# Performance work log

Measured on AMD Instinct MI355X. Metric: run time of the kernel, lower is better.

Reference implementation:

```python
import jax, jax.numpy as jnp
import numpy as np

N = 1024      # node_dim
D = 1024      # initial_dim (== node_dim so all QRs are square)
B = 8         # batch_dim
L = 4         # layer_dim
DEG = 16      # out-degree per node
E = N * DEG


def setup_inputs() -> dict:
    key = jax.random.key(0)
    k1, k2 = jax.random.split(key)
    x0 = jax.random.normal(k1, (B, N, D), dtype=jnp.float32)
    # every node appears as a source exactly DEG times -> degree > 0 everywhere
    src = jnp.repeat(jnp.arange(N, dtype=jnp.int64), DEG)
    dst = jax.random.randint(k2, (E,), 0, N, dtype=jnp.int64)
    edge_index = jnp.stack([src, dst], axis=1)
    return {"x0": x0, "edge_index": edge_index, "run": 1}


def _rfp_conv(x, src, dst, deg):
    # x: [N, D]; one RFPConv application on a single graph signal
    inv_sqrt = deg ** -0.5                               # deg^{-1/2}
    w = inv_sqrt[src] * inv_sqrt[dst]                    # [E]
    msg = w[:, None] * x[dst]                            # gathered + normalized neighbour feats
    agg = 0.5 * jax.ops.segment_sum(msg, src, num_segments=N)
    # unsorted_segment_mean(deg[src]*x[src], src) == sum / count, count = deg
    src_term = deg[src][:, None] * x[src]
    mean = jax.ops.segment_sum(src_term, src, num_segments=N) / jnp.maximum(deg, 1.0)[:, None]
    agg = agg + 0.5 * mean                               # [N, D]
    # D == N so reduced QR == complete (full_matrices=True) QR
    return jnp.linalg.qr(agg)[0]


def reference(x0, edge_index, run):
    if not run:
        return None
    src = edge_index[:, 0]
    dst = edge_index[:, 1]
    deg = jax.ops.segment_sum(jnp.ones((E,), jnp.float32), src, num_segments=N)
    conv = jax.vmap(lambda x: _rfp_conv(x, src, dst, deg))
    traj = [x0]
    for i in range(L):
        traj.append(conv(traj[i]))
    return jnp.concatenate(traj, axis=-1)  # [B, N, D + L*N]
```

## Files before the change

kernel.cpp:

```cpp
#include <hip/hip_runtime.h>
#include <cmath>

#define NN 1024
#define DD 1024
#define BB 8
#define LL 4
#define OUTD (DD*(LL+1))
#define NB 32
#define NPAN 32
#define BSTR ((size_t)NN*OUTD)
#define VSTR 540672ull

typedef short b8v __attribute__((ext_vector_type(8)));
typedef float f4v __attribute__((ext_vector_type(4)));

__device__ __forceinline__ unsigned short f2bf(float x){
  unsigned u=__float_as_uint(x);
  return (unsigned short)((u + 0x7FFFu + ((u>>16)&1u))>>16);
}
__device__ __forceinline__ float bf2f(unsigned short h){
  return __uint_as_float(((unsigned)h)<<16);
}
__device__ __forceinline__ void bsplit3(float x, short& h, short& m, short& l){
  unsigned short hh=f2bf(x);
  float r1=x-bf2f(hh);
  unsigned short mm=f2bf(r1);
  float r2=r1-bf2f(mm);
  h=(short)hh; m=(short)mm; l=(short)f2bf(r2);
}
__device__ __forceinline__ f4v mfma6(b8v ah,b8v am,b8v al,b8v bh,b8v bm,b8v bl,f4v acc){
  acc=__builtin_amdgcn_mfma_f32_16x16x32_bf16(al,bh,acc,0,0,0);
  acc=__builtin_amdgcn_mfma_f32_16x16x32_bf16(ah,bl,acc,0,0,0);
  acc=__builtin_amdgcn_mfma_f32_16x16x32_bf16(am,bm,acc,0,0,0);
  acc=__builtin_amdgcn_mfma_f32_16x16x32_bf16(am,bh,acc,0,0,0);
  acc=__builtin_amdgcn_mfma_f32_16x16x32_bf16(ah,bm,acc,0,0,0);
  acc=__builtin_amdgcn_mfma_f32_16x16x32_bf16(ah,bh,acc,0,0,0);
  return acc;
}
__device__ __forceinline__ size_t voff(int kb){
  return 32768ull*(size_t)kb - 512ull*(size_t)kb*(size_t)(kb-1);
}

__device__ __forceinline__ void wait_flag(int* f){
  if(threadIdx.x==0){
    while(__hip_atomic_load(f, __ATOMIC_RELAXED, __HIP_MEMORY_SCOPE_AGENT)==0)
      __builtin_amdgcn_s_sleep(8);
    __threadfence();
  }
  __syncthreads();
}
__device__ __forceinline__ void set_flag(int* f){
  __syncthreads();
  if(threadIdx.x==0)
    __hip_atomic_store(f, 1, __ATOMIC_RELEASE, __HIP_MEMORY_SCOPE_AGENT);
}

__global__ void k_init(float* degF, int* flags){
  degF[threadIdx.x]=0.f;
  flags[threadIdx.x]=0;
}

__global__ void k_deg(const int* __restrict__ ei, float* __restrict__ degF, int E){
  int e=blockIdx.x*blockDim.x+threadIdx.x;
  if(e<E) atomicAdd(&degF[ei[2*e]],1.f);
}

__global__ void k_scan(const float* __restrict__ degF, float* __restrict__ isq, int* __restrict__ rowoff){
  __shared__ int s[NN];
  int i=threadIdx.x;
  int d=(int)degF[i];
  s[i]=d; __syncthreads();
  for(int off=1;off<NN;off<<=1){
    int v=(i>=off)?s[i-off]:0;
    __syncthreads();
    s[i]+=v;
    __syncthreads();
  }
  if(i==0) rowoff[0]=0;
  rowoff[i+1]=s[i];
  isq[i]=(d>0)?(float)(1.0/sqrt((double)d)):0.f;
}

__global__ void k_copyx0(const float* __restrict__ x0, float* __restrict__ out){
  size_t t=(size_t)blockIdx.x*blockDim.x+threadIdx.x;
  if(t>=(size_t)BB*NN*DD) return;
  int d=(int)(t&(DD-1)); size_t bn=t>>10;
  out[bn*OUTD+d]=x0[t];
}

__global__ void k_conv(const float* __restrict__ xin, const int* __restrict__ ei,
                       const float* __restrict__ degF, const float* __restrict__ isq,
                       const int* __restrict__ rowoff, float* Aout){
  int i=blockIdx.x, b=blockIdx.y;
  __shared__ int sdst[64]; __shared__ float sw[64];
  int r0=rowoff[i], r1=rowoff[i+1];
  int cnt=r1-r0; if(cnt>64) cnt=64;
  float di=degF[i], isqi=isq[i];
  for(int e=threadIdx.x;e<cnt;e+=blockDim.x){
    int dv=ei[2*(r0+e)+1];
    sdst[e]=dv; sw[e]=isqi*isq[dv];
  }
  __syncthreads();
  float cm=((float)(r1-r0))*di/fmaxf(di,1.f);
  const float* xi=xin+((size_t)(b*NN+i))*OUTD;
  float* ao=Aout+((size_t)(b*NN+i))*OUTD;
  for(int d=threadIdx.x; d<DD; d+=blockDim.x){
    float acc=0.f;
    for(int e=0;e<cnt;e++) acc+=sw[e]*xin[((size_t)(b*NN+sdst[e]))*OUTD+d];
    ao[d]=0.5f*acc+0.5f*cm*xi[d];
  }
}

template<int MQ>
__device__ __forceinline__ void panel_factor2(float (&p)[MQ], int mq, int m,
    short* __restrict__ vh, short* __restrict__ vm2, short* __restrict__ vl,
    float* __restrict__ Twslot, char* SM){
  float* vsh2=(float*)SM;
  float (*Ssav)[33]=(float(*)[33])(SM+8192);
  float* taus=(float*)(SM+12416);
  int tid=threadIdx.x, c=tid>>4, rw=tid&15;
  #pragma unroll 1
  for(int j=0;j<NB;j++){
    float* vb=vsh2+((j&1)<<10);
    if(c==j){
      float ss=0.f, al=0.f;
      #pragma unroll
      for(int q=0;q<MQ;q++) if(q<mq){
        int r=rw+(q<<4);
        float pv=p[q];
        if(r>j) ss+=pv*pv; else if(r==j) al=pv;
      }
      #pragma unroll
      for(int o=8;o>0;o>>=1){ ss+=__shfl_xor(ss,o,16); al+=__shfl_xor(al,o,16); }
      float tau,scale;
      if(ss==0.f){ tau=0.f; scale=0.f; }
      else{
        double bn=sqrt((double)al*(double)al+(double)ss);
        float beta=(al>=0.f)?(float)(-bn):(float)bn;
        tau=(beta-al)/beta; scale=1.f/(al-beta);
      }
      #pragma unroll
      for(int q=0;q<MQ;q++) if(q<mq){
        int r=rw+(q<<4);
        if(r>j){ p[q]*=scale; vb[r]=p[q]; }
        else if(r==j) vb[r]=1.f;
      }
      if(rw==0) taus[j]=tau;
    }
    __syncthreads();
    float tau=taus[j];
    float sc=0.f;
    #pragma unroll
    for(int q=0;q<MQ;q++) if(q<mq){
      int r=rw+(q<<4);
      if(r>=j) sc+=vb[r]*p[q];
    }
    #pragma unroll
    for(int o=8;o>0;o>>=1) sc+=__shfl_xor(sc,o,16);
    if(c>j){
      float wv=tau*sc;
      #pragma unroll
      for(int q=0;q<MQ;q++) if(q<mq){
        int r=rw+(q<<4);
        if(r>=j) p[q]-=wv*vb[r];
      }
    } else if(c<j && rw==0) Ssav[j][c]=sc;
  }
  __syncthreads();
  float tq0=0.f,tq1=0.f;
  #pragma unroll
  for(int j=0;j<32;j++){
    float tj=taus[j];
    float s=((rw<j)?tq0*Ssav[j][rw]:0.f)+((rw+16<j)?tq1*Ssav[j][rw+16]:0.f);
    #pragma unroll
    for(int o=8;o>0;o>>=1) s+=__shfl_xor(s,o,16);
    float val=-tj*s;
    if(j>c){ if((j&15)==rw){ if(j<16) tq0=val; else tq1=val; } }
    else if(j==c){ if((j&15)==rw){ if(j<16) tq0=tj; else tq1=tj; } }
  }
  Twslot[(c<<5)+rw]=tq0;
  Twslot[(c<<5)+rw+16]=tq1;
  #pragma unroll
  for(int q=0;q<MQ;q++) if(q<mq){
    int r=rw+(q<<4);
    float v=(r>c)?p[q]:((r==c)?1.f:0.f);
    short h,mi,lo; bsplit3(v,h,mi,lo);
    size_t o2=(size_t)c*m+r;
    vh[o2]=h; vm2[o2]=mi; vl[o2]=lo;
  }
  __syncthreads();
}

template<int MQ>
__device__ __forceinline__ void panel_phase(float* __restrict__ Ab, int c0, int m,
    short* __restrict__ vh, short* __restrict__ vm2, short* __restrict__ vl,
    float* __restrict__ Tw, char* SM){
  int tid=threadIdx.x, c=tid>>4, rw=tid&15;
  int mq=m>>4;
  float p[MQ];
  #pragma unroll
  for(int q=0;q<MQ;q++){
    p[q]=0.f;
    if(q<mq){ int r=rw+(q<<4); p[q]=Ab[(size_t)(c0+r)*OUTD+c0+c]; }
  }
  panel_factor2<MQ>(p,mq,m,vh,vm2,vl,Tw,SM);
}

template<bool TRANS>
__device__ void blk_update(float* __restrict__ Ab,
    const short* __restrict__ vh, const short* __restrict__ vm2, const short* __restrict__ vl,
    const float* __restrict__ Tb, int k0, int c0, char* SM){
  float (*Tsh)[33]=(float(*)[33])(SM);
  float (*Wt)[33] =(float(*)[33])(SM+4224);
  float (*Wp)[32][33]=(float(*)[32][33])(SM+8448);
  short (*W2h)[40]=(short(*)[40])(SM+8448);
  short (*W2m)[40]=(short(*)[40])(SM+11008);
  short (*W2l)[40]=(short(*)[40])(SM+13568);
  int tid=threadIdx.x, w=tid>>6, lane=tid&63, lr=lane&15, lq=lane>>4;
  int m=NN-k0;
  for(int idx=tid; idx<1024; idx+=512) Tsh[idx>>5][idx&31]=Tb[idx];
  int jt=w&1, ct=(w>>1)&1, kh=w>>2;
  int ja=jt*16+lr, cb=ct*16+lr;
  int ko=(kh<<5)+(lq<<3);
  const short* ph=vh +(size_t)ja*m;
  const short* pm=vm2+(size_t)ja*m;
  const short* pl=vl +(size_t)ja*m;
  const float* sp0=Ab+(size_t)k0*OUTD + c0+cb;
  f4v acc={0.f,0.f,0.f,0.f};
  const b8v zz={0,0,0,0,0,0,0,0};
  b8v ah=zz,amv=zz,alv=zz; float sv[8];
  #pragma unroll
  for(int e=0;e<8;e++) sv[e]=0.f;
  if(ko<m){
    ah=*(const b8v*)(ph+ko); amv=*(const b8v*)(pm+ko); alv=*(const b8v*)(pl+ko);
    const float* sp=sp0+(size_t)ko*OUTD;
    #pragma unroll
    for(int e=0;e<8;e++) sv[e]=sp[(size_t)e*OUTD];
  }
  for(int rt=0; rt<m; rt+=64){
    b8v nh=zz,nm=zz,nl=zz; float nsv[8];
    #pragma unroll
    for(int e=0;e<8;e++) nsv[e]=0.f;
    int nk=rt+64+ko;
    if(nk<m){
      nh=*(const b8v*)(ph+nk); nm=*(const b8v*)(pm+nk); nl=*(const b8v*)(pl+nk);
      const float* sp=sp0+(size_t)nk*OUTD;
      #pragma unroll
      for(int e=0;e<8;e++) nsv[e]=sp[(size_t)e*OUTD];
    }
    b8v bh,bm2,bl2;
    #pragma unroll
    for(int e=0;e<8;e++){ short h,mi,lo; bsplit3(sv[e],h,mi,lo); bh[e]=h; bm2[e]=mi; bl2[e]=lo; }
    acc=mfma6(ah,amv,alv,bh,bm2,bl2,acc);
    ah=nh; amv=nm; alv=nl;
    #pragma unroll
    for(int e=0;e<8;e++) sv[e]=nsv[e];
  }
  #pragma unroll
  for(int i=0;i<4;i++) Wp[kh][jt*16+4*lq+i][ct*16+lr]=acc[i];
  __syncthreads();
  #pragma unroll
  for(int s=0;s<2;s++){
    int idx=tid+(s<<9), j=idx>>5, cc=idx&31;
    Wt[j][cc]=Wp[0][j][cc]+Wp[1][j][cc];
  }
  __syncthreads();
  float w2r[2];
  #pragma unroll
  for(int s=0;s<2;s++){
    int idx=tid+(s<<9), cc=idx>>5, j=idx&31;
    float s2=0.f;
    if(TRANS){ for(int q=0;q<=j;q++) s2+=Tsh[q][j]*Wt[q][cc]; }
    else     { for(int q=j;q<32;q++) s2+=Tsh[j][q]*Wt[q][cc]; }
    w2r[s]=s2;
  }
  __syncthreads();
  #pragma unroll
  for(int s=0;s<2;s++){
    int idx=tid+(s<<9), cc=idx>>5, j=idx&31;
    short h,mi,lo; bsplit3(w2r[s],h,mi,lo);
    W2h[cc][j]=h; W2m[cc][j]=mi; W2l[cc][j]=lo;
  }
  __syncthreads();
  int rt4=w&3, ct2=w>>2;
  int cb2=ct2*16+lr;
  b8v wh=*(const b8v*)&W2h[cb2][lq<<3];
  b8v wm=*(const b8v*)&W2m[cb2][lq<<3];
  b8v wl2=*(const b8v*)&W2l[cb2][lq<<3];
  int ccol=c0+cb2;
  for(int rt=0; rt<m; rt+=64){
    int rbase=rt+rt4*16;
    if(rbase<m){
      float oldv[4];
      #pragma unroll
      for(int i=0;i<4;i++) oldv[i]=Ab[(size_t)(k0+rbase+4*lq+i)*OUTD+ccol];
      b8v ah2,am3,al3;
      #pragma unroll
      for(int e=0;e<8;e++){
        size_t o2=(size_t)(8*lq+e)*m + rbase+lr;
        ah2[e]=vh[o2]; am3[e]=vm2[o2]; al3[e]=vl[o2];
      }
      f4v a2={0.f,0.f,0.f,0.f};
      a2=mfma6(ah2,am3,al3,wh,wm,wl2,a2);
      #pragma unroll
      for(int i=0;i<4;i++)
        Ab[(size_t)(k0+rbase+4*lq+i)*OUTD+ccol]=oldv[i]-a2[i];
    }
  }
  __syncthreads();
}

__global__ __launch_bounds__(512) void k_layer(float* A, short* vTh, short* vTm, short* vTl,
                                               float* Tws, int* flags){
  __shared__ __align__(16) char SM[16896];
  int bid=blockIdx.x, tid=threadIdx.x;
  int b=bid>>5, j=bid&31;
  float* Ab=A+(size_t)b*BSTR;
  short* vhb=vTh+(size_t)b*VSTR;
  short* vmb=vTm+(size_t)b*VSTR;
  short* vlb=vTl+(size_t)b*VSTR;
  float* Tb =Tws+(size_t)b*NPAN*1024;
  int* fb=flags+(b<<5);
  int c0=j<<5;

  for(int kb=0; kb<j; kb++){
    wait_flag(&fb[kb]);
    size_t vo=voff(kb);
    blk_update<true>(Ab, vhb+vo, vmb+vo, vlb+vo, Tb+(size_t)kb*1024, kb<<5, c0, SM);
  }
  {
    int m=NN-c0;
    size_t vo=voff(j);
    float* Tw=Tb+(size_t)j*1024;
    if(j<8)       panel_phase<64>(Ab,c0,m, vhb+vo,vmb+vo,vlb+vo, Tw, SM);
    else if(j<16) panel_phase<48>(Ab,c0,m, vhb+vo,vmb+vo,vlb+vo, Tw, SM);
    else if(j<24) panel_phase<32>(Ab,c0,m, vhb+vo,vmb+vo,vlb+vo, Tw, SM);
    else          panel_phase<16>(Ab,c0,m, vhb+vo,vmb+vo,vlb+vo, Tw, SM);
    set_flag(&fb[j]);
  }
  for(int idx=tid; idx<NN*32; idx+=512){
    int r=idx>>5, cc=idx&31;
    Ab[(size_t)r*OUTD+c0+cc]=(r==c0+cc)?1.f:0.f;
  }
  __syncthreads();
  for(int kb=j; kb>=0; kb--){
    size_t vo=voff(kb);
    blk_update<false>(Ab, vhb+vo, vmb+vo, vlb+vo, Tb+(size_t)kb*1024, kb<<5, c0, SM);
  }
}

extern "C" void kernel_launch(void* const* d_in, const int* in_sizes, int n_in,
                              void* d_out, int out_size, void* d_ws, size_t ws_size,
                              hipStream_t stream){
  const float* x0=(const float*)d_in[0];
  const int* ei=(const int*)d_in[1];
  int E=in_sizes[1]/2;
  float* out=(float*)d_out;
  float* W=(float*)d_ws;
  float* degF=W;
  float* isq =W+1024;
  int*  rowoff=(int*)(W+2048);
  int*  flags =(int*)(W+2048)+1040;
  float* Tws  =W+4352;
  short* vTh  =(short*)(Tws+262144);
  short* vTm  =vTh+(size_t)BB*VSTR;
  short* vTl  =vTm+(size_t)BB*VSTR;

  size_t tot=(size_t)BB*NN*DD;
  k_init<<<1,1024,0,stream>>>(degF,flags);
  k_deg<<<(E+255)/256,256,0,stream>>>(ei,degF,E);
  k_scan<<<1,NN,0,stream>>>(degF,isq,rowoff);
  k_copyx0<<<(int)((tot+255)/256),256,0,stream>>>(x0,out);

  for(int l=0;l<LL;l++){
    float* A=out+(size_t)(l+1)*DD;
    k_conv<<<dim3(NN,BB),256,0,stream>>>(out+(size_t)l*DD,ei,degF,isq,rowoff,A);
    int* fl=flags+l*256;
    void* kargs[]={(void*)&A,(void*)&vTh,(void*)&vTm,(void*)&vTl,(void*)&Tws,(void*)&fl};
    hipLaunchCooperativeKernel(reinterpret_cast<void*>(k_layer),
                               dim3(256),dim3(512),kargs,0,stream);
  }
}
```

Baseline: 15.79 ms.

## Fuse conv and QR layers into one persistent kernel with LDS-resident column slabs

Replaces the per-layer conv kernel and cooperative QR kernel with a single cooperative megakernel. Each block holds its 1024x32 column slab in LDS across all four layers and does the graph convolution on that slab locally, since the conv mixes rows only and columns stay independent. Edge weights are precomputed once. Panel factorisation and the blocked Householder updates now read and write LDS instead of global memory, and grid.sync separates layers. The cost is about 148KB of LDS per block, which limits occupancy to one block per CU, plus a grid-wide barrier per layer.

```diff
diff --git a/kernel.cpp b/kernel.cpp
--- a/kernel.cpp
+++ b/kernel.cpp
@@ -1,15 +1,16 @@
 #include <hip/hip_runtime.h>
+#include <hip/hip_cooperative_groups.h>
 #include <cmath>
 
+namespace cg = cooperative_groups;
+
 #define NN 1024
-#define DD 1024
 #define BB 8
 #define LL 4
-#define OUTD (DD*(LL+1))
+#define OUTD 5120
 #define NB 32
-#define NPAN 32
-#define BSTR ((size_t)NN*OUTD)
 #define VSTR 540672ull
+#define SMBYTES 152064
 
 typedef short b8v __attribute__((ext_vector_type(8)));
 typedef float f4v __attribute__((ext_vector_type(4)));
@@ -59,12 +60,10 @@
   degF[threadIdx.x]=0.f;
   flags[threadIdx.x]=0;
 }
-
 __global__ void k_deg(const int* __restrict__ ei, float* __restrict__ degF, int E){
   int e=blockIdx.x*blockDim.x+threadIdx.x;
   if(e<E) atomicAdd(&degF[ei[2*e]],1.f);
 }
-
 __global__ void k_scan(const float* __restrict__ degF, float* __restrict__ isq, int* __restrict__ rowoff){
   __shared__ int s[NN];
   int i=threadIdx.x;
@@ -80,142 +79,55 @@
   rowoff[i+1]=s[i];
   isq[i]=(d>0)?(float)(1.0/sqrt((double)d)):0.f;
 }
-
-__global__ void k_copyx0(const float* __restrict__ x0, float* __restrict__ out){
-  size_t t=(size_t)blockIdx.x*blockDim.x+threadIdx.x;
-  if(t>=(size_t)BB*NN*DD) return;
-  int d=(int)(t&(DD-1)); size_t bn=t>>10;
-  out[bn*OUTD+d]=x0[t];
-}
-
-__global__ void k_conv(const float* __restrict__ xin, const int* __restrict__ ei,
-                       const float* __restrict__ degF, const float* __restrict__ isq,
-                       const int* __restrict__ rowoff, float* Aout){
-  int i=blockIdx.x, b=blockIdx.y;
-  __shared__ int sdst[64]; __shared__ float sw[64];
-  int r0=rowoff[i], r1=rowoff[i+1];
-  int cnt=r1-r0; if(cnt>64) cnt=64;
-  float di=degF[i], isqi=isq[i];
-  for(int e=threadIdx.x;e<cnt;e+=blockDim.x){
-    int dv=ei[2*(r0+e)+1];
-    sdst[e]=dv; sw[e]=isqi*isq[dv];
-  }
-  __syncthreads();
-  float cm=((float)(r1-r0))*di/fmaxf(di,1.f);
-  const float* xi=xin+((size_t)(b*NN+i))*OUTD;
-  float* ao=Aout+((size_t)(b*NN+i))*OUTD;
-  for(int d=threadIdx.x; d<DD; d+=blockDim.x){
-    float acc=0.f;
-    for(int e=0;e<cnt;e++) acc+=sw[e]*xin[((size_t)(b*NN+sdst[e]))*OUTD+d];
-    ao[d]=0.5f*acc+0.5f*cm*xi[d];
-  }
-}
-
-template<int MQ>
-__device__ __forceinline__ void panel_factor2(float (&p)[MQ], int mq, int m,
-    short* __restrict__ vh, short* __restrict__ vm2, short* __restrict__ vl,
-    float* __restrict__ Twslot, char* SM){
-  float* vsh2=(float*)SM;
-  float (*Ssav)[33]=(float(*)[33])(SM+8192);
-  float* taus=(float*)(SM+12416);
-  int tid=threadIdx.x, c=tid>>4, rw=tid&15;
-  #pragma unroll 1
-  for(int j=0;j<NB;j++){
-    float* vb=vsh2+((j&1)<<10);
-    if(c==j){
-      float ss=0.f, al=0.f;
-      #pragma unroll
-      for(int q=0;q<MQ;q++) if(q<mq){
-        int r=rw+(q<<4);
-        float pv=p[q];
-        if(r>j) ss+=pv*pv; else if(r==j) al=pv;
-      }
-      #pragma unroll
-      for(int o=8;o>0;o>>=1){ ss+=__shfl_xor(ss,o,16); al+=__shfl_xor(al,o,16); }
-      float tau,scale;
-      if(ss==0.f){ tau=0.f; scale=0.f; }
-      else{
-        double bn=sqrt((double)al*(double)al+(double)ss);
-        float beta=(al>=0.f)?(float)(-bn):(float)bn;
-        tau=(beta-al)/beta; scale=1.f/(al-beta);
-      }
-      #pragma unroll
-      for(int q=0;q<MQ;q++) if(q<mq){
-        int r=rw+(q<<4);
-        if(r>j){ p[q]*=scale; vb[r]=p[q]; }
-        else if(r==j) vb[r]=1.f;
-      }
-      if(rw==0) taus[j]=tau;
-    }
-    __syncthreads();
-    float tau=taus[j];
-    float sc=0.f;
-    #pragma unroll
-    for(int q=0;q<MQ;q++) if(q<mq){
-      int r=rw+(q<<4);
-      if(r>=j) sc+=vb[r]*p[q];
-    }
-    #pragma unroll
-    for(int o=8;o>0;o>>=1) sc+=__shfl_xor(sc,o,16);
-    if(c>j){
-      float wv=tau*sc;
-      #pragma unroll
-      for(int q=0;q<MQ;q++) if(q<mq){
-        int r=rw+(q<<4);
-        if(r>=j) p[q]-=wv*vb[r];
-      }
-    } else if(c<j && rw==0) Ssav[j][c]=sc;
-  }
-  __syncthreads();
-  float tq0=0.f,tq1=0.f;
-  #pragma unroll
-  for(int j=0;j<32;j++){
-    float tj=taus[j];
-    float s=((rw<j)?tq0*Ssav[j][rw]:0.f)+((rw+16<j)?tq1*Ssav[j][rw+16]:0.f);
-    #pragma unroll
-    for(int o=8;o>0;o>>=1) s+=__shfl_xor(s,o,16);
-    float val=-tj*s;
-    if(j>c){ if((j&15)==rw){ if(j<16) tq0=val; else tq1=val; } }
-    else if(j==c){ if((j&15)==rw){ if(j<16) tq0=tj; else tq1=tj; } }
-  }
-  Twslot[(c<<5)+rw]=tq0;
-  Twslot[(c<<5)+rw+16]=tq1;
-  #pragma unroll
-  for(int q=0;q<MQ;q++) if(q<mq){
-    int r=rw+(q<<4);
-    float v=(r>c)?p[q]:((r==c)?1.f:0.f);
-    short h,mi,lo; bsplit3(v,h,mi,lo);
-    size_t o2=(size_t)c*m+r;
-    vh[o2]=h; vm2[o2]=mi; vl[o2]=lo;
-  }
-  __syncthreads();
-}
-
-template<int MQ>
-__device__ __forceinline__ void panel_phase(float* __restrict__ Ab, int c0, int m,
-    short* __restrict__ vh, short* __restrict__ vm2, short* __restrict__ vl,
-    float* __restrict__ Tw, char* SM){
-  int tid=threadIdx.x, c=tid>>4, rw=tid&15;
-  int mq=m>>4;
-  float p[MQ];
-  #pragma unroll
-  for(int q=0;q<MQ;q++){
-    p[q]=0.f;
-    if(q<mq){ int r=rw+(q<<4); p[q]=Ab[(size_t)(c0+r)*OUTD+c0+c]; }
-  }
-  panel_factor2<MQ>(p,mq,m,vh,vm2,vl,Tw,SM);
+__global__ void k_sw(const int* __restrict__ ei, const float* __restrict__ isq,
+                     float* __restrict__ swv, int E){
+  int e=blockIdx.x*blockDim.x+threadIdx.x;
+  if(e<E) swv[e]=isq[ei[2*e]]*isq[ei[2*e+1]];
+}
+
+__device__ void conv_S(float (*S)[33], const int* __restrict__ ei,
+                       const float* __restrict__ swv, const float* __restrict__ degF,
+                       const int* __restrict__ rowoff){
+  int tid=threadIdx.x;
+  int ra=2*tid, rb=2*tid+1;
+  int e0=rowoff[ra], e1=rowoff[rb], e2=rowoff[rb+1];
+  float a0[32], a1[32];
+  #pragma unroll
+  for(int c=0;c<32;c++){ a0[c]=0.f; a1[c]=0.f; }
+  for(int e=e0;e<e1;e++){
+    int dv=ei[2*e+1]; float w=swv[e];
+    #pragma unroll
+    for(int c=0;c<32;c++) a0[c]+=w*S[dv][c];
+  }
+  for(int e=e1;e<e2;e++){
+    int dv=ei[2*e+1]; float w=swv[e];
+    #pragma unroll
+    for(int c=0;c<32;c++) a1[c]+=w*S[dv][c];
+  }
+  float d0=degF[ra], d1=degF[rb];
+  float cm0=(float)(e1-e0)*d0/fmaxf(d0,1.f);
+  float cm1=(float)(e2-e1)*d1/fmaxf(d1,1.f);
+  #pragma unroll
+  for(int c=0;c<32;c++){
+    a0[c]=0.5f*a0[c]+0.5f*cm0*S[ra][c];
+    a1[c]=0.5f*a1[c]+0.5f*cm1*S[rb][c];
+  }
+  __syncthreads();
+  #pragma unroll
+  for(int c=0;c<32;c++){ S[ra][c]=a0[c]; S[rb][c]=a1[c]; }
+  __syncthreads();
 }
 
 template<bool TRANS>
-__device__ void blk_update(float* __restrict__ Ab,
+__device__ void apply_S(float (*S)[33], char* SC,
     const short* __restrict__ vh, const short* __restrict__ vm2, const short* __restrict__ vl,
-    const float* __restrict__ Tb, int k0, int c0, char* SM){
-  float (*Tsh)[33]=(float(*)[33])(SM);
-  float (*Wt)[33] =(float(*)[33])(SM+4224);
-  float (*Wp)[32][33]=(float(*)[32][33])(SM+8448);
-  short (*W2h)[40]=(short(*)[40])(SM+8448);
-  short (*W2m)[40]=(short(*)[40])(SM+11008);
-  short (*W2l)[40]=(short(*)[40])(SM+13568);
+    const float* __restrict__ Tb, int k0){
+  float (*Tsh)[33]=(float(*)[33])(SC);
+  float (*Wt)[33] =(float(*)[33])(SC+4224);
+  float (*Wp)[32][33]=(float(*)[32][33])(SC+8448);
+  short (*W2h)[40]=(short(*)[40])(SC+8448);
+  short (*W2m)[40]=(short(*)[40])(SC+11008);
+  short (*W2l)[40]=(short(*)[40])(SC+13568);
   int tid=threadIdx.x, w=tid>>6, lane=tid&63, lr=lane&15, lq=lane>>4;
   int m=NN-k0;
   for(int idx=tid; idx<1024; idx+=512) Tsh[idx>>5][idx&31]=Tb[idx];
@@ -225,36 +137,28 @@
   const short* ph=vh +(size_t)ja*m;
   const short* pm=vm2+(size_t)ja*m;
   const short* pl=vl +(size_t)ja*m;
-  const float* sp0=Ab+(size_t)k0*OUTD + c0+cb;
   f4v acc={0.f,0.f,0.f,0.f};
   const b8v zz={0,0,0,0,0,0,0,0};
-  b8v ah=zz,amv=zz,alv=zz; float sv[8];
-  #pragma unroll
-  for(int e=0;e<8;e++) sv[e]=0.f;
-  if(ko<m){
-    ah=*(const b8v*)(ph+ko); amv=*(const b8v*)(pm+ko); alv=*(const b8v*)(pl+ko);
-    const float* sp=sp0+(size_t)ko*OUTD;
-    #pragma unroll
-    for(int e=0;e<8;e++) sv[e]=sp[(size_t)e*OUTD];
-  }
+  b8v ah=zz,amv=zz,alv=zz;
+  if(ko<m){ ah=*(const b8v*)(ph+ko); amv=*(const b8v*)(pm+ko); alv=*(const b8v*)(pl+ko); }
   for(int rt=0; rt<m; rt+=64){
-    b8v nh=zz,nm=zz,nl=zz; float nsv[8];
-    #pragma unroll
-    for(int e=0;e<8;e++) nsv[e]=0.f;
-    int nk=rt+64+ko;
-    if(nk<m){
-      nh=*(const b8v*)(ph+nk); nm=*(const b8v*)(pm+nk); nl=*(const b8v*)(pl+nk);
-      const float* sp=sp0+(size_t)nk*OUTD;
-      #pragma unroll
-      for(int e=0;e<8;e++) nsv[e]=sp[(size_t)e*OUTD];
+    int kk=rt+ko;
+    b8v nh=zz,nm=zz,nl=zz;
+    int nk=kk+64;
+    if(nk<m){ nh=*(const b8v*)(ph+nk); nm=*(const b8v*)(pm+nk); nl=*(const b8v*)(pl+nk); }
+    float sv[8];
+    if(kk<m){
+      #pragma unroll
+      for(int e=0;e<8;e++) sv[e]=S[k0+kk+e][cb];
+    } else {
+      #pragma unroll
+      for(int e=0;e<8;e++) sv[e]=0.f;
     }
     b8v bh,bm2,bl2;
     #pragma unroll
     for(int e=0;e<8;e++){ short h,mi,lo; bsplit3(sv[e],h,mi,lo); bh[e]=h; bm2[e]=mi; bl2[e]=lo; }
     acc=mfma6(ah,amv,alv,bh,bm2,bl2,acc);
     ah=nh; amv=nm; alv=nl;
-    #pragma unroll
-    for(int e=0;e<8;e++) sv[e]=nsv[e];
   }
   #pragma unroll
   for(int i=0;i<4;i++) Wp[kh][jt*16+4*lq+i][ct*16+lr]=acc[i];
@@ -287,13 +191,12 @@
   b8v wh=*(const b8v*)&W2h[cb2][lq<<3];
   b8v wm=*(const b8v*)&W2m[cb2][lq<<3];
   b8v wl2=*(const b8v*)&W2l[cb2][lq<<3];
-  int ccol=c0+cb2;
   for(int rt=0; rt<m; rt+=64){
     int rbase=rt+rt4*16;
     if(rbase<m){
       float oldv[4];
       #pragma unroll
-      for(int i=0;i<4;i++) oldv[i]=Ab[(size_t)(k0+rbase+4*lq+i)*OUTD+ccol];
+      for(int i=0;i<4;i++) oldv[i]=S[k0+rbase+4*lq+i][cb2];
       b8v ah2,am3,al3;
       #pragma unroll
       for(int e=0;e<8;e++){
@@ -304,48 +207,153 @@
       a2=mfma6(ah2,am3,al3,wh,wm,wl2,a2);
       #pragma unroll
       for(int i=0;i<4;i++)
-        Ab[(size_t)(k0+rbase+4*lq+i)*OUTD+ccol]=oldv[i]-a2[i];
-    }
-  }
-  __syncthreads();
-}
-
-__global__ __launch_bounds__(512) void k_layer(float* A, short* vTh, short* vTm, short* vTl,
-                                               float* Tws, int* flags){
-  __shared__ __align__(16) char SM[16896];
+        S[k0+rbase+4*lq+i][cb2]=oldv[i]-a2[i];
+    }
+  }
+  __syncthreads();
+}
+
+template<int MQ>
+__device__ __forceinline__ void panel_S(float (*S)[33], char* SC, int c0, int m,
+    short* __restrict__ vh, short* __restrict__ vm2, short* __restrict__ vl,
+    float* __restrict__ Tw){
+  float (*Ssav)[33]=(float(*)[33])(SC);
+  float* taus=(float*)(SC+4224);
+  int tid=threadIdx.x, c=tid>>4, rw=tid&15;
+  int mq=m>>4;
+  float p[MQ];
+  #pragma unroll
+  for(int q=0;q<MQ;q++){
+    p[q]=0.f;
+    if(q<mq) p[q]=S[c0+rw+(q<<4)][c];
+  }
+  __syncthreads();
+  #pragma unroll 1
+  for(int j=0;j<NB;j++){
+    if(c==j){
+      float ss=0.f, al=0.f;
+      #pragma unroll
+      for(int q=0;q<MQ;q++) if(q<mq){
+        int r=rw+(q<<4);
+        float pv=p[q];
+        if(r>j) ss+=pv*pv; else if(r==j) al=pv;
+      }
+      #pragma unroll
+      for(int o=8;o>0;o>>=1){ ss+=__shfl_xor(ss,o,16); al+=__shfl_xor(al,o,16); }
+      float tau,scale;
+      if(ss==0.f){ tau=0.f; scale=0.f; }
+      else{
+        double bn=sqrt((double)al*(double)al+(double)ss);
+        float beta=(al>=0.f)?(float)(-bn):(float)bn;
+        tau=(beta-al)/beta; scale=1.f/(al-beta);
+      }
+      #pragma unroll
+      for(int q=0;q<MQ;q++) if(q<mq){
+        int r=rw+(q<<4);
+        if(r>j){ p[q]*=scale; S[c0+r][j]=p[q]; }
+        else if(r==j) S[c0+r][j]=1.f;
+      }
+      if(rw==0) taus[j]=tau;
+    }
+    __syncthreads();
+    float tau=taus[j];
+    float sc=0.f;
+    #pragma unroll
+    for(int q=0;q<MQ;q++) if(q<mq){
+      int r=rw+(q<<4);
+      if(r>=j) sc+=S[c0+r][j]*p[q];
+    }
+    #pragma unroll
+    for(int o=8;o>0;o>>=1) sc+=__shfl_xor(sc,o,16);
+    if(c>j){
+      float wv=tau*sc;
+      #pragma unroll
+      for(int q=0;q<MQ;q++) if(q<mq){
+        int r=rw+(q<<4);
+        if(r>=j) p[q]-=wv*S[c0+r][j];
+      }
+    } else if(c<j && rw==0) Ssav[j][c]=sc;
+  }
+  __syncthreads();
+  float tq0=0.f,tq1=0.f;
+  #pragma unroll
+  for(int jj=0;jj<32;jj++){
+    float tj=taus[jj];
+    float s=((rw<jj)?tq0*Ssav[jj][rw]:0.f)+((rw+16<jj)?tq1*Ssav[jj][rw+16]:0.f);
+    #pragma unroll
+    for(int o=8;o>0;o>>=1) s+=__shfl_xor(s,o,16);
+    float val=-tj*s;
+    if(jj>c){ if((jj&15)==rw){ if(jj<16) tq0=val; else tq1=val; } }
+    else if(jj==c){ if((jj&15)==rw){ if(jj<16) tq0=tj; else tq1=tj; } }
+  }
+  Tw[(c<<5)+rw]=tq0;
+  Tw[(c<<5)+rw+16]=tq1;
+  #pragma unroll
+  for(int q=0;q<MQ;q++) if(q<mq){
+    int r=rw+(q<<4);
+    float v=(r>c)?p[q]:((r==c)?1.f:0.f);
+    short h,mi,lo; bsplit3(v,h,mi,lo);
+    size_t o2=(size_t)c*m+r;
+    vh[o2]=h; vm2[o2]=mi; vl[o2]=lo;
+  }
+  __syncthreads();
+}
+
+__global__ __launch_bounds__(512) void k_mega(const float* __restrict__ x0, float* __restrict__ out,
+    const int* __restrict__ ei, const float* __restrict__ swv,
+    const float* __restrict__ degF, const int* __restrict__ rowoff,
+    short* vTh, short* vTm, short* vTl, float* Tws, int* flags){
+  cg::grid_group grid = cg::this_grid();
+  extern __shared__ char SMEM[];
+  float (*S)[33]=(float(*)[33])SMEM;
+  char* SC=SMEM+135168;
   int bid=blockIdx.x, tid=threadIdx.x;
-  int b=bid>>5, j=bid&31;
-  float* Ab=A+(size_t)b*BSTR;
+  int b=bid>>5, j=bid&31, c0=j<<5;
   short* vhb=vTh+(size_t)b*VSTR;
   short* vmb=vTm+(size_t)b*VSTR;
   short* vlb=vTl+(size_t)b*VSTR;
-  float* Tb =Tws+(size_t)b*NPAN*1024;
-  int* fb=flags+(b<<5);
-  int c0=j<<5;
-
-  for(int kb=0; kb<j; kb++){
-    wait_flag(&fb[kb]);
-    size_t vo=voff(kb);
-    blk_update<true>(Ab, vhb+vo, vmb+vo, vlb+vo, Tb+(size_t)kb*1024, kb<<5, c0, SM);
-  }
-  {
-    int m=NN-c0;
-    size_t vo=voff(j);
-    float* Tw=Tb+(size_t)j*1024;
-    if(j<8)       panel_phase<64>(Ab,c0,m, vhb+vo,vmb+vo,vlb+vo, Tw, SM);
-    else if(j<16) panel_phase<48>(Ab,c0,m, vhb+vo,vmb+vo,vlb+vo, Tw, SM);
-    else if(j<24) panel_phase<32>(Ab,c0,m, vhb+vo,vmb+vo,vlb+vo, Tw, SM);
-    else          panel_phase<16>(Ab,c0,m, vhb+vo,vmb+vo,vlb+vo, Tw, SM);
-    set_flag(&fb[j]);
-  }
+  float* Tb=Tws+((size_t)b<<15);
+
   for(int idx=tid; idx<NN*32; idx+=512){
     int r=idx>>5, cc=idx&31;
-    Ab[(size_t)r*OUTD+c0+cc]=(r==c0+cc)?1.f:0.f;
-  }
-  __syncthreads();
-  for(int kb=j; kb>=0; kb--){
-    size_t vo=voff(kb);
-    blk_update<false>(Ab, vhb+vo, vmb+vo, vlb+vo, Tb+(size_t)kb*1024, kb<<5, c0, SM);
+    float v=x0[(((size_t)b*NN+r)<<10)+c0+cc];
+    S[r][cc]=v;
+    out[((size_t)b*NN+r)*OUTD + c0+cc]=v;
+  }
+  __syncthreads();
+
+  for(int l=0;l<LL;l++){
+    int* fl=flags+((l*BB+b)<<5);
+    conv_S(S,ei,swv,degF,rowoff);
+    for(int kb=0;kb<j;kb++){
+      wait_flag(&fl[kb]);
+      size_t vo=voff(kb);
+      apply_S<true>(S,SC,vhb+vo,vmb+vo,vlb+vo,Tb+((size_t)kb<<10),kb<<5);
+    }
+    {
+      int m=NN-c0;
+      size_t vo=voff(j);
+      float* Tw=Tb+((size_t)j<<10);
+      if(j<8)       panel_S<64>(S,SC,c0,m,vhb+vo,vmb+vo,vlb+vo,Tw);
+      else if(j<16) panel_S<48>(S,SC,c0,m,vhb+vo,vmb+vo,vlb+vo,Tw);
+      else if(j<24) panel_S<32>(S,SC,c0,m,vhb+vo,vmb+vo,vlb+vo,Tw);
+      else          panel_S<16>(S,SC,c0,m,vhb+vo,vmb+vo,vlb+vo,Tw);
+      set_flag(&fl[j]);
+    }
+    for(int idx=tid; idx<NN*32; idx+=512){
+      int r=idx>>5, cc=idx&31;
+      S[r][cc]=(r==c0+cc)?1.f:0.f;
+    }
+    __syncthreads();
+    for(int kb=j;kb>=0;kb--){
+      size_t vo=voff(kb);
+      apply_S<false>(S,SC,vhb+vo,vmb+vo,vlb+vo,Tb+((size_t)kb<<10),kb<<5);
+    }
+    for(int idx=tid; idx<NN*32; idx+=512){
+      int r=idx>>5, cc=idx&31;
+      out[((size_t)b*NN+r)*OUTD+(size_t)(l+1)*1024 + c0+cc]=S[r][cc];
+    }
+    grid.sync();
   }
 }
 
@@ -361,23 +369,22 @@
   float* isq =W+1024;
   int*  rowoff=(int*)(W+2048);
   int*  flags =(int*)(W+2048)+1040;
-  float* Tws  =W+4352;
-  short* vTh  =(short*)(Tws+262144);
+  float* swv  =W+4352;
+  float* Tws  =W+20736;
+  short* vTh  =(short*)(W+282880);
   short* vTm  =vTh+(size_t)BB*VSTR;
   short* vTl  =vTm+(size_t)BB*VSTR;
 
-  size_t tot=(size_t)BB*NN*DD;
+  (void)hipFuncSetAttribute(reinterpret_cast<const void*>(&k_mega),
+                            hipFuncAttributeMaxDynamicSharedMemorySize, SMBYTES);
+
   k_init<<<1,1024,0,stream>>>(degF,flags);
   k_deg<<<(E+255)/256,256,0,stream>>>(ei,degF,E);
   k_scan<<<1,NN,0,stream>>>(degF,isq,rowoff);
-  k_copyx0<<<(int)((tot+255)/256),256,0,stream>>>(x0,out);
-
-  for(int l=0;l<LL;l++){
-    float* A=out+(size_t)(l+1)*DD;
-    k_conv<<<dim3(NN,BB),256,0,stream>>>(out+(size_t)l*DD,ei,degF,isq,rowoff,A);
-    int* fl=flags+l*256;
-    void* kargs[]={(void*)&A,(void*)&vTh,(void*)&vTm,(void*)&vTl,(void*)&Tws,(void*)&fl};
-    hipLaunchCooperativeKernel(reinterpret_cast<void*>(k_layer),
-                               dim3(256),dim3(512),kargs,0,stream);
-  }
-}
+  k_sw<<<(E+255)/256,256,0,stream>>>(ei,isq,swv,E);
+
+  void* kargs[]={(void*)&x0,(void*)&out,(void*)&ei,(void*)&swv,(void*)&degF,
+                 (void*)&rowoff,(void*)&vTh,(void*)&vTm,(void*)&vTl,(void*)&Tws,(void*)&flags};
+  hipLaunchCooperativeKernel(reinterpret_cast<void*>(k_mega),
+                             dim3(256),dim3(512),kargs,SMBYTES,stream);
+}
```

After: 14.83 ms. 6.1% less time.
